# Optimization experiments

Hardware: AMD Instinct MI355X
Metric: run time of the kernel (lower is better)

## Reference

```python
import jax, jax.numpy as jnp
import numpy as np
import math

N_ITERS = 10
N_SPIXELS = 256
NEG_INF = -1e10


def _grid_layout(h, w, n_spixels):
    # init_grid: near-square superpixel grid
    nw = int(math.sqrt(n_spixels * w / h))
    nh = int(math.sqrt(n_spixels * h / w))
    cy = np.minimum((np.arange(h) * nh) // h, nh - 1)
    cx = np.minimum((np.arange(w) * nw) // w, nw - 1)
    iy = np.broadcast_to(cy[:, None], (h, w))
    ix = np.broadcast_to(cx[None, :], (h, w))
    init_idx = iy * nw + ix  # [h,w] hard grid assignment
    # 9 candidate superpixels per pixel (3x3 neighborhood of its grid cell)
    offs = np.array([(dy, dx) for dy in (-1, 0, 1) for dx in (-1, 0, 1)])
    ny = iy[None] + offs[:, 0, None, None]  # [9,h,w]
    nx = ix[None] + offs[:, 1, None, None]
    valid = (ny >= 0) & (ny < nh) & (nx >= 0) & (nx < nw)
    nidx = np.clip(ny, 0, nh - 1) * nw + np.clip(nx, 0, nw - 1)
    return init_idx.astype(np.int32), nidx.astype(np.int32), valid, nw, nh


def setup_inputs() -> dict:
    key = jax.random.key(0)
    x = jax.random.normal(key, (2, 20, 512, 512), dtype=jnp.float32)
    return {"x": x}


def reference(x):
    b, c, h, w = x.shape
    init_idx_np, nidx_np, valid_np, nw, nh = _grid_layout(h, w, N_SPIXELS)
    K = nw * nh
    n = h * w
    init_idx = jnp.asarray(init_idx_np.reshape(n))          # [N]
    nidx = jnp.asarray(nidx_np.reshape(9, n))                # [9,N]
    valid = jnp.asarray(valid_np.reshape(9, n))              # [9,N]
    flat_nidx = nidx.reshape(-1)                             # [9N]

    pf_all = x.reshape(b, c, n)

    def init_spf(pf):  # pf [c,N] -> [c,K]: hard-assignment mean (InitSpixelFeats)
        s = jax.ops.segment_sum(pf.T, init_idx, num_segments=K)      # [K,c]
        cnt = jax.ops.segment_sum(jnp.ones((n,), pf.dtype), init_idx, num_segments=K)
        return (s / jnp.maximum(cnt, 1.0)[:, None]).T

    def calc_neg_dist(pf, spf):  # CalcAssoc: [9,N] neg sq dist to 9 neighbors
        nf = spf[:, nidx]                                    # [c,9,N]
        d = jnp.sum((pf[:, None, :] - nf) ** 2, axis=0)      # [9,N]
        return jnp.where(valid, -d, NEG_INF)

    def map_p2sp(pf, Q):  # CalcSpixelFeats: Q-weighted scatter mean, Q [9,N]
        wf = (pf[:, None, :] * Q[None]).reshape(c, -1)       # [c,9N]
        num = jax.ops.segment_sum(wf.T, flat_nidx, num_segments=K)   # [K,c]
        den = jax.ops.segment_sum(Q.reshape(-1), flat_nidx, num_segments=K)
        return (num / jnp.maximum(den, 1e-8)[:, None]).T

    def per_sample(pf):
        spf0 = init_spf(jax.lax.stop_gradient(pf))  # spf init from detached pf
        Q0 = jnp.zeros((9, n), pf.dtype)
        def body(carry, _):
            spf, _ = carry
            Q = jax.nn.softmax(calc_neg_dist(pf, spf), axis=0)
            return (map_p2sp(pf, Q), Q), None
        (spf, Q), _ = jax.lax.scan(body, (spf0, Q0), None, length=N_ITERS)
        return Q, spf

    Q, spf = jax.vmap(per_sample)(pf_all)
    return Q.reshape(b, 9, h, w), spf, x
```

## Files before the change

### kernel.cpp

```cpp
#include <hip/hip_runtime.h>

#define BATCH 2
#define C 20
#define H 512
#define W 512
#define NPIX (H*W)
#define NW 16
#define NH 16
#define K 256
#define NITERS 10
#define SPLIT 4
#define PITCH 260
#define NEG_INF_F (-1.0e10f)
#define PART_STRIDE 189

__global__ __launch_bounds__(256)
void ssn_init_kernel(const float* __restrict__ x,
                     float* __restrict__ outX,
                     float* __restrict__ wpart) {
    __shared__ float pf_tile[C][PITCH];
    __shared__ float chpart[80];
    int t = threadIdx.x;
    int bi = blockIdx.x;
    int s    = bi & 3;
    int cell = (bi >> 2) & (K - 1);
    int b    = bi >> 10;
    int ky = cell >> 4, kx = cell & 15;
    int py = t >> 5, px = t & 31;
    int y  = ky * 32 + s * 8 + py;
    int xx = kx * 32 + px;

    const float* xb = x    + (size_t)b * C * NPIX + y * W + xx;
    float*       ox = outX + (size_t)b * C * NPIX + y * W + xx;
#pragma unroll
    for (int ch = 0; ch < C; ++ch) {
        float v = xb[(size_t)ch * NPIX];
        ox[(size_t)ch * NPIX] = v;
        pf_tile[ch][t] = v;
    }
    __syncthreads();
    if (t < 80) {
        int ch = t >> 2, q = t & 3;
        const float4* p = (const float4*)&pf_tile[ch][0];
        float s4 = 0.f;
#pragma unroll
        for (int i = 0; i < 16; ++i) {
            float4 v = p[q * 16 + i];
            s4 += v.x + v.y + v.z + v.w;
        }
        chpart[t] = s4;
    }
    __syncthreads();
    if (t < PART_STRIDE) {
        float v = 0.f;
        if (t >= 84 && t < 104) {
            int ch = t - 84;
            v = chpart[ch * 4] + chpart[ch * 4 + 1]
              + chpart[ch * 4 + 2] + chpart[ch * 4 + 3];
        } else if (t == 104) {
            v = 256.0f;
        }
        wpart[(size_t)(b * K + cell) * (SPLIT * PART_STRIDE)
              + s * PART_STRIDE + t] = v;
    }
}

__global__ void ssn_reduce_kernel(const float* __restrict__ part,
                                  float* __restrict__ spf,
                                  float* __restrict__ outSpf,
                                  int final_mode) {
    int idx = blockIdx.x * blockDim.x + threadIdx.x;
    if (idx >= BATCH * K * C) return;
    int ch = idx % C;
    int k  = (idx / C) % K;
    int b  = idx / (C * K);
    int ky = k >> 4, kx = k & 15;
    float num = 0.f, den = 0.f;
#pragma unroll
    for (int j2 = 0; j2 < 9; ++j2) {
        int cy = ky - (j2 / 3 - 1), cx = kx - (j2 % 3 - 1);
        if (cy >= 0 && cy < NH && cx >= 0 && cx < NW) {
            const float* p = part +
                (size_t)(b * K + cy * NW + cx) * (SPLIT * PART_STRIDE) + j2 * 21;
#pragma unroll
            for (int ss = 0; ss < SPLIT; ++ss) {
                num += p[ss * PART_STRIDE + ch];
                den += p[ss * PART_STRIDE + 20];
            }
        }
    }
    float v = num / fmaxf(den, 1e-8f);
    if (final_mode) outSpf[(b * C + ch) * K + k] = v;
    else            spf[(b * K + k) * C + ch]    = v;
}

__global__ __launch_bounds__(256)
void ssn_iterate_kernel(const float* __restrict__ x,
                        const float* __restrict__ spf,
                        float* __restrict__ wpart,
                        float* __restrict__ outQ,
                        int last) {
    __shared__ float spf_lds[9][C];
    __shared__ float sumsq_lds[9];
    __shared__ float pf_tile[C + 1][PITCH];
    __shared__ float w_tile[9][PITCH];

    int t = threadIdx.x;
    int bi = blockIdx.x;
    int s    = bi & 3;
    int cell = (bi >> 2) & (K - 1);
    int b    = bi >> 10;
    int ky = cell >> 4, kx = cell & 15;

    int py = t >> 5, px = t & 31;
    int y  = ky * 32 + s * 8 + py;
    int xx = kx * 32 + px;

    float pf[C];
    const float* xb = x + (size_t)b * C * NPIX + y * W + xx;
#pragma unroll
    for (int ch = 0; ch < C; ++ch) pf[ch] = xb[(size_t)ch * NPIX];

    if (t < 9 * C) {
        int jj = t / C, ch = t % C;
        int ny = ky + jj / 3 - 1, nx = kx + jj % 3 - 1;
        float v = 0.f;
        if (ny >= 0 && ny < NH && nx >= 0 && nx < NW)
            v = spf[(size_t)(b * K + ny * NW + nx) * C + ch];
        spf_lds[jj][ch] = v;
    }
    if (t < 9) {
        int ny = ky + t / 3 - 1, nx = kx + t % 3 - 1;
        float ss2 = 0.f;
        if (ny >= 0 && ny < NH && nx >= 0 && nx < NW) {
            const float* sp = spf + (size_t)(b * K + ny * NW + nx) * C;
#pragma unroll
            for (int ch = 0; ch < C; ++ch) ss2 += sp[ch] * sp[ch];
        }
        sumsq_lds[t] = ss2;
    }
    __syncthreads();

    float sc[9];
#pragma unroll
    for (int j = 0; j < 9; ++j) {
        int ny = ky + j / 3 - 1, nx = kx + j % 3 - 1;
        bool valid = (ny >= 0 && ny < NH && nx >= 0 && nx < NW);
        float dot = 0.f;
#pragma unroll
        for (int ch = 0; ch < C; ++ch) dot = fmaf(pf[ch], spf_lds[j][ch], dot);
        sc[j] = valid ? fmaf(2.f, dot, -sumsq_lds[j]) : NEG_INF_F;
    }
    float m = sc[0];
#pragma unroll
    for (int j = 1; j < 9; ++j) m = fmaxf(m, sc[j]);
    float wv[9], wsum = 0.f;
#pragma unroll
    for (int j = 0; j < 9; ++j) { wv[j] = __expf(sc[j] - m); wsum += wv[j]; }
    float inv = 1.0f / wsum;
#pragma unroll
    for (int j = 0; j < 9; ++j) { wv[j] *= inv; w_tile[j][t] = wv[j]; }
#pragma unroll
    for (int ch = 0; ch < C; ++ch) pf_tile[ch][t] = pf[ch];
    pf_tile[C][t] = 1.0f;

    if (last) {
        float* q = outQ + (size_t)b * 9 * NPIX + y * W + xx;
#pragma unroll
        for (int j = 0; j < 9; ++j) q[(size_t)j * NPIX] = wv[j];
    }
    __syncthreads();

    if (t < 144) {
        int tile = t >> 4;
        int lane = t & 15;
        int jt = tile / 3;
        int rt = tile % 3;
        float acc[3][7];
#pragma unroll
        for (int jj = 0; jj < 3; ++jj)
#pragma unroll
            for (int rr = 0; rr < 7; ++rr) acc[jj][rr] = 0.f;

#pragma unroll
        for (int cc = 0; cc < 4; ++cc) {
            int c4 = lane + (cc << 4);
            float4 w4[3], f4[7];
#pragma unroll
            for (int jj = 0; jj < 3; ++jj)
                w4[jj] = ((const float4*)&w_tile[3 * jt + jj][0])[c4];
#pragma unroll
            for (int rr = 0; rr < 7; ++rr)
                f4[rr] = ((const float4*)&pf_tile[7 * rt + rr][0])[c4];
#pragma unroll
            for (int jj = 0; jj < 3; ++jj)
#pragma unroll
                for (int rr = 0; rr < 7; ++rr) {
                    acc[jj][rr] = fmaf(w4[jj].x, f4[rr].x, acc[jj][rr]);
                    acc[jj][rr] = fmaf(w4[jj].y, f4[rr].y, acc[jj][rr]);
                    acc[jj][rr] = fmaf(w4[jj].z, f4[rr].z, acc[jj][rr]);
                    acc[jj][rr] = fmaf(w4[jj].w, f4[rr].w, acc[jj][rr]);
                }
        }
#pragma unroll
        for (int off = 8; off >= 1; off >>= 1)
#pragma unroll
            for (int jj = 0; jj < 3; ++jj)
#pragma unroll
                for (int rr = 0; rr < 7; ++rr)
                    acc[jj][rr] += __shfl_down(acc[jj][rr], off);
        if (lane == 0) {
            float* dst = wpart + (size_t)(b * K + cell) * (SPLIT * PART_STRIDE)
                       + s * PART_STRIDE;
#pragma unroll
            for (int jj = 0; jj < 3; ++jj)
#pragma unroll
                for (int rr = 0; rr < 7; ++rr)
                    dst[(3 * jt + jj) * 21 + 7 * rt + rr] = acc[jj][rr];
        }
    }
}

extern "C" void kernel_launch(void* const* d_in, const int* in_sizes, int n_in,
                              void* d_out, int out_size, void* d_ws, size_t ws_size,
                              hipStream_t stream) {
    const float* x = (const float*)d_in[0];
    float* out = (float*)d_out;
    float* outQ   = out;
    float* outSpf = out + (size_t)BATCH * 9 * NPIX;
    float* outX   = outSpf + (size_t)BATCH * C * K;

    float* ws   = (float*)d_ws;
    float* spf  = ws;
    float* part = spf + (size_t)BATCH * K * C;

    ssn_init_kernel<<<BATCH * K * SPLIT, 256, 0, stream>>>(x, outX, part);
    ssn_reduce_kernel<<<160, 64, 0, stream>>>(part, spf, nullptr, 0);

    for (int it = 0; it < NITERS; ++it) {
        ssn_iterate_kernel<<<BATCH * K * SPLIT, 256, 0, stream>>>(
            x, spf, part, outQ, (it == NITERS - 1) ? 1 : 0);
        if (it < NITERS - 1)
            ssn_reduce_kernel<<<160, 64, 0, stream>>>(part, spf, nullptr, 0);
    }
    ssn_reduce_kernel<<<160, 64, 0, stream>>>(part, nullptr, outSpf, 1);
}
```

Before: 255.5 us.

## Fuse spixel reduction into iterate kernel via atomics and triple-buffered partials

Removes the separate reduce kernel between iterations. Each iterate block now gathers the 9x9 neighbour partial sums and divides them itself to rebuild its superpixel features. Split blocks accumulate into one record per cell with atomicAdd, and a rotating triple buffer lets each pass zero the buffer used two passes later. The init kernel now covers a whole cell per block, and the final kernel reads a single record instead of four splits. This saves about nine launches and a global round trip per iteration, at the cost of redundant gather work in every block and atomic contention.

```diff
diff --git a/kernel.cpp b/kernel.cpp
--- a/kernel.cpp
+++ b/kernel.cpp
@@ -2,42 +2,50 @@
 
 #define BATCH 2
 #define C 20
-#define H 512
 #define W 512
-#define NPIX (H*W)
+#define NPIX (512*512)
 #define NW 16
 #define NH 16
 #define K 256
 #define NITERS 10
-#define SPLIT 4
 #define PITCH 260
 #define NEG_INF_F (-1.0e10f)
-#define PART_STRIDE 189
+#define REC 189
 
 __global__ __launch_bounds__(256)
 void ssn_init_kernel(const float* __restrict__ x,
                      float* __restrict__ outX,
-                     float* __restrict__ wpart) {
+                     float* __restrict__ bufA,
+                     float* __restrict__ bufB) {
     __shared__ float pf_tile[C][PITCH];
     __shared__ float chpart[80];
-    int t = threadIdx.x;
-    int bi = blockIdx.x;
-    int s    = bi & 3;
-    int cell = (bi >> 2) & (K - 1);
-    int b    = bi >> 10;
-    int ky = cell >> 4, kx = cell & 15;
-    int py = t >> 5, px = t & 31;
-    int y  = ky * 32 + s * 8 + py;
-    int xx = kx * 32 + px;
-
-    const float* xb = x    + (size_t)b * C * NPIX + y * W + xx;
-    float*       ox = outX + (size_t)b * C * NPIX + y * W + xx;
-#pragma unroll
-    for (int ch = 0; ch < C; ++ch) {
-        float v = xb[(size_t)ch * NPIX];
-        ox[(size_t)ch * NPIX] = v;
-        pf_tile[ch][t] = v;
-    }
+    const int t    = threadIdx.x;
+    const int bi   = blockIdx.x;
+    const int cell = bi & (K - 1);
+    const int b    = bi >> 8;
+    const int ky = cell >> 4, kx = cell & 15;
+    const int py = t >> 5, px = t & 31;
+    const int xcol = kx * 32 + px;
+
+    const float* xb = x    + (size_t)b * C * NPIX;
+    float*       ox = outX + (size_t)b * C * NPIX;
+    float sum4[C];
+#pragma unroll
+    for (int ch = 0; ch < C; ++ch) sum4[ch] = 0.f;
+#pragma unroll
+    for (int p = 0; p < 4; ++p) {
+        int y = ky * 32 + p * 8 + py;
+        const float* src = xb + (size_t)y * W + xcol;
+        float*       dst = ox + (size_t)y * W + xcol;
+#pragma unroll
+        for (int ch = 0; ch < C; ++ch) {
+            float v = src[(size_t)ch * NPIX];
+            sum4[ch] += v;
+            dst[(size_t)ch * NPIX] = v;
+        }
+    }
+#pragma unroll
+    for (int ch = 0; ch < C; ++ch) pf_tile[ch][t] = sum4[ch];
     __syncthreads();
     if (t < 80) {
         int ch = t >> 2, q = t & 3;
@@ -51,24 +59,181 @@
         chpart[t] = s4;
     }
     __syncthreads();
-    if (t < PART_STRIDE) {
+    if (t < REC) {
         float v = 0.f;
         if (t >= 84 && t < 104) {
             int ch = t - 84;
             v = chpart[ch * 4] + chpart[ch * 4 + 1]
               + chpart[ch * 4 + 2] + chpart[ch * 4 + 3];
         } else if (t == 104) {
-            v = 256.0f;
-        }
-        wpart[(size_t)(b * K + cell) * (SPLIT * PART_STRIDE)
-              + s * PART_STRIDE + t] = v;
-    }
-}
-
-__global__ void ssn_reduce_kernel(const float* __restrict__ part,
-                                  float* __restrict__ spf,
-                                  float* __restrict__ outSpf,
-                                  int final_mode) {
+            v = 1024.0f;
+        }
+        bufA[(size_t)bi * REC + t] = v;
+        bufB[(size_t)bi * REC + t] = 0.f;
+    }
+}
+
+__global__ __launch_bounds__(256)
+void ssn_iterate_kernel(const float* __restrict__ x,
+                        const float* __restrict__ rp,
+                        float* __restrict__ wp,
+                        float* __restrict__ zp,
+                        float* __restrict__ outQ,
+                        int last) {
+    __shared__ float spf_lds[9][C];
+    __shared__ float den_lds[9];
+    __shared__ float sumsq_lds[9];
+    __shared__ float pf_tile[C][PITCH];
+    __shared__ float w_tile[9][PITCH];
+
+    const int t  = threadIdx.x;
+    const int bi = blockIdx.x;
+    const int s    = bi & 3;
+    const int cell = (bi >> 2) & (K - 1);
+    const int b    = bi >> 10;
+    const int bcell = (b << 8) + cell;
+    const int ky = cell >> 4, kx = cell & 15;
+    const int py = t >> 5, px = t & 31;
+    const int y  = ky * 32 + s * 8 + py;
+    const int xcol = kx * 32 + px;
+
+    if (s == 0 && t < REC) zp[(size_t)bcell * REC + t] = 0.f;
+
+    float pf[C];
+    const float* xb = x + (size_t)b * C * NPIX + (size_t)y * W + xcol;
+#pragma unroll
+    for (int ch = 0; ch < C; ++ch) pf[ch] = xb[(size_t)ch * NPIX];
+
+    float numreg = 0.f;
+    if (t < 180) {
+        int jj = t / 20, ch = t % 20;
+        int ny = ky + jj / 3 - 1, nx = kx + jj % 3 - 1;
+        if (ny >= 0 && ny < NH && nx >= 0 && nx < NW) {
+#pragma unroll
+            for (int j2 = 0; j2 < 9; ++j2) {
+                int cy = ny - (j2 / 3 - 1), cx = nx - (j2 % 3 - 1);
+                if (cy >= 0 && cy < NH && cx >= 0 && cx < NW)
+                    numreg += rp[(size_t)((b << 8) + cy * NW + cx) * REC
+                                 + j2 * 21 + ch];
+            }
+        }
+    }
+    if (t >= 192 && t < 201) {
+        int jj = t - 192;
+        int ny = ky + jj / 3 - 1, nx = kx + jj % 3 - 1;
+        float den = 0.f;
+        if (ny >= 0 && ny < NH && nx >= 0 && nx < NW) {
+#pragma unroll
+            for (int j2 = 0; j2 < 9; ++j2) {
+                int cy = ny - (j2 / 3 - 1), cx = nx - (j2 % 3 - 1);
+                if (cy >= 0 && cy < NH && cx >= 0 && cx < NW)
+                    den += rp[(size_t)((b << 8) + cy * NW + cx) * REC
+                              + j2 * 21 + 20];
+            }
+        }
+        den_lds[jj] = den;
+    }
+    __syncthreads();
+    if (t < 180) {
+        int jj = t / 20, ch = t % 20;
+        spf_lds[jj][ch] = numreg / fmaxf(den_lds[jj], 1e-8f);
+    }
+    __syncthreads();
+    if (t < 9) {
+        float ss2 = 0.f;
+#pragma unroll
+        for (int ch = 0; ch < C; ++ch) ss2 += spf_lds[t][ch] * spf_lds[t][ch];
+        sumsq_lds[t] = ss2;
+    }
+    __syncthreads();
+
+    float sc[9];
+#pragma unroll
+    for (int j = 0; j < 9; ++j) {
+        int ny = ky + j / 3 - 1, nx = kx + j % 3 - 1;
+        bool valid = (ny >= 0 && ny < NH && nx >= 0 && nx < NW);
+        float dot = 0.f;
+#pragma unroll
+        for (int ch = 0; ch < C; ++ch) dot = fmaf(pf[ch], spf_lds[j][ch], dot);
+        sc[j] = valid ? fmaf(2.f, dot, -sumsq_lds[j]) : NEG_INF_F;
+    }
+    float m = sc[0];
+#pragma unroll
+    for (int j = 1; j < 9; ++j) m = fmaxf(m, sc[j]);
+    float wv[9], wsum = 0.f;
+#pragma unroll
+    for (int j = 0; j < 9; ++j) { wv[j] = __expf(sc[j] - m); wsum += wv[j]; }
+    float inv = 1.0f / wsum;
+#pragma unroll
+    for (int j = 0; j < 9; ++j) { wv[j] *= inv; w_tile[j][t] = wv[j]; }
+#pragma unroll
+    for (int ch = 0; ch < C; ++ch) pf_tile[ch][t] = pf[ch];
+
+    if (last) {
+        float* q = outQ + (size_t)b * 9 * NPIX + (size_t)y * W + xcol;
+#pragma unroll
+        for (int j = 0; j < 9; ++j) q[(size_t)j * NPIX] = wv[j];
+    }
+    __syncthreads();
+
+    if (t < 144) {
+        const int tile = t >> 4, lane = t & 15;
+        const int jt = tile / 3, rt = tile % 3;
+        float acc[3][7];
+#pragma unroll
+        for (int jj = 0; jj < 3; ++jj)
+#pragma unroll
+            for (int rr = 0; rr < 7; ++rr) acc[jj][rr] = 0.f;
+
+#pragma unroll
+        for (int cc = 0; cc < 4; ++cc) {
+            int c4 = lane + (cc << 4);
+            float4 w4[3], f4[7];
+#pragma unroll
+            for (int jj = 0; jj < 3; ++jj)
+                w4[jj] = ((const float4*)&w_tile[3 * jt + jj][0])[c4];
+#pragma unroll
+            for (int rr = 0; rr < 7; ++rr) {
+                int r = 7 * rt + rr;
+                if (r < 20) f4[rr] = ((const float4*)&pf_tile[r][0])[c4];
+            }
+#pragma unroll
+            for (int jj = 0; jj < 3; ++jj)
+#pragma unroll
+                for (int rr = 0; rr < 7; ++rr) {
+                    int r = 7 * rt + rr;
+                    if (r < 20) {
+                        acc[jj][rr] = fmaf(w4[jj].x, f4[rr].x, acc[jj][rr]);
+                        acc[jj][rr] = fmaf(w4[jj].y, f4[rr].y, acc[jj][rr]);
+                        acc[jj][rr] = fmaf(w4[jj].z, f4[rr].z, acc[jj][rr]);
+                        acc[jj][rr] = fmaf(w4[jj].w, f4[rr].w, acc[jj][rr]);
+                    } else {
+                        acc[jj][rr] += w4[jj].x + w4[jj].y
+                                     + w4[jj].z + w4[jj].w;
+                    }
+                }
+        }
+#pragma unroll
+        for (int off = 8; off >= 1; off >>= 1)
+#pragma unroll
+            for (int jj = 0; jj < 3; ++jj)
+#pragma unroll
+                for (int rr = 0; rr < 7; ++rr)
+                    acc[jj][rr] += __shfl_down(acc[jj][rr], off);
+        if (lane == 0) {
+            float* dst = wp + (size_t)bcell * REC;
+#pragma unroll
+            for (int jj = 0; jj < 3; ++jj)
+#pragma unroll
+                for (int rr = 0; rr < 7; ++rr)
+                    atomicAdd(&dst[(3 * jt + jj) * 21 + 7 * rt + rr],
+                              acc[jj][rr]);
+        }
+    }
+}
+
+__global__ void ssn_final_kernel(const float* __restrict__ rec,
+                                 float* __restrict__ outSpf) {
     int idx = blockIdx.x * blockDim.x + threadIdx.x;
     if (idx >= BATCH * K * C) return;
     int ch = idx % C;
@@ -80,145 +245,13 @@
     for (int j2 = 0; j2 < 9; ++j2) {
         int cy = ky - (j2 / 3 - 1), cx = kx - (j2 % 3 - 1);
         if (cy >= 0 && cy < NH && cx >= 0 && cx < NW) {
-            const float* p = part +
-                (size_t)(b * K + cy * NW + cx) * (SPLIT * PART_STRIDE) + j2 * 21;
-#pragma unroll
-            for (int ss = 0; ss < SPLIT; ++ss) {
-                num += p[ss * PART_STRIDE + ch];
-                den += p[ss * PART_STRIDE + 20];
-            }
-        }
-    }
-    float v = num / fmaxf(den, 1e-8f);
-    if (final_mode) outSpf[(b * C + ch) * K + k] = v;
-    else            spf[(b * K + k) * C + ch]    = v;
-}
-
-__global__ __launch_bounds__(256)
-void ssn_iterate_kernel(const float* __restrict__ x,
-                        const float* __restrict__ spf,
-                        float* __restrict__ wpart,
-                        float* __restrict__ outQ,
-                        int last) {
-    __shared__ float spf_lds[9][C];
-    __shared__ float sumsq_lds[9];
-    __shared__ float pf_tile[C + 1][PITCH];
-    __shared__ float w_tile[9][PITCH];
-
-    int t = threadIdx.x;
-    int bi = blockIdx.x;
-    int s    = bi & 3;
-    int cell = (bi >> 2) & (K - 1);
-    int b    = bi >> 10;
-    int ky = cell >> 4, kx = cell & 15;
-
-    int py = t >> 5, px = t & 31;
-    int y  = ky * 32 + s * 8 + py;
-    int xx = kx * 32 + px;
-
-    float pf[C];
-    const float* xb = x + (size_t)b * C * NPIX + y * W + xx;
-#pragma unroll
-    for (int ch = 0; ch < C; ++ch) pf[ch] = xb[(size_t)ch * NPIX];
-
-    if (t < 9 * C) {
-        int jj = t / C, ch = t % C;
-        int ny = ky + jj / 3 - 1, nx = kx + jj % 3 - 1;
-        float v = 0.f;
-        if (ny >= 0 && ny < NH && nx >= 0 && nx < NW)
-            v = spf[(size_t)(b * K + ny * NW + nx) * C + ch];
-        spf_lds[jj][ch] = v;
-    }
-    if (t < 9) {
-        int ny = ky + t / 3 - 1, nx = kx + t % 3 - 1;
-        float ss2 = 0.f;
-        if (ny >= 0 && ny < NH && nx >= 0 && nx < NW) {
-            const float* sp = spf + (size_t)(b * K + ny * NW + nx) * C;
-#pragma unroll
-            for (int ch = 0; ch < C; ++ch) ss2 += sp[ch] * sp[ch];
-        }
-        sumsq_lds[t] = ss2;
-    }
-    __syncthreads();
-
-    float sc[9];
-#pragma unroll
-    for (int j = 0; j < 9; ++j) {
-        int ny = ky + j / 3 - 1, nx = kx + j % 3 - 1;
-        bool valid = (ny >= 0 && ny < NH && nx >= 0 && nx < NW);
-        float dot = 0.f;
-#pragma unroll
-        for (int ch = 0; ch < C; ++ch) dot = fmaf(pf[ch], spf_lds[j][ch], dot);
-        sc[j] = valid ? fmaf(2.f, dot, -sumsq_lds[j]) : NEG_INF_F;
-    }
-    float m = sc[0];
-#pragma unroll
-    for (int j = 1; j < 9; ++j) m = fmaxf(m, sc[j]);
-    float wv[9], wsum = 0.f;
-#pragma unroll
-    for (int j = 0; j < 9; ++j) { wv[j] = __expf(sc[j] - m); wsum += wv[j]; }
-    float inv = 1.0f / wsum;
-#pragma unroll
-    for (int j = 0; j < 9; ++j) { wv[j] *= inv; w_tile[j][t] = wv[j]; }
-#pragma unroll
-    for (int ch = 0; ch < C; ++ch) pf_tile[ch][t] = pf[ch];
-    pf_tile[C][t] = 1.0f;
-
-    if (last) {
-        float* q = outQ + (size_t)b * 9 * NPIX + y * W + xx;
-#pragma unroll
-        for (int j = 0; j < 9; ++j) q[(size_t)j * NPIX] = wv[j];
-    }
-    __syncthreads();
-
-    if (t < 144) {
-        int tile = t >> 4;
-        int lane = t & 15;
-        int jt = tile / 3;
-        int rt = tile % 3;
-        float acc[3][7];
-#pragma unroll
-        for (int jj = 0; jj < 3; ++jj)
-#pragma unroll
-            for (int rr = 0; rr < 7; ++rr) acc[jj][rr] = 0.f;
-
-#pragma unroll
-        for (int cc = 0; cc < 4; ++cc) {
-            int c4 = lane + (cc << 4);
-            float4 w4[3], f4[7];
-#pragma unroll
-            for (int jj = 0; jj < 3; ++jj)
-                w4[jj] = ((const float4*)&w_tile[3 * jt + jj][0])[c4];
-#pragma unroll
-            for (int rr = 0; rr < 7; ++rr)
-                f4[rr] = ((const float4*)&pf_tile[7 * rt + rr][0])[c4];
-#pragma unroll
-            for (int jj = 0; jj < 3; ++jj)
-#pragma unroll
-                for (int rr = 0; rr < 7; ++rr) {
-                    acc[jj][rr] = fmaf(w4[jj].x, f4[rr].x, acc[jj][rr]);
-                    acc[jj][rr] = fmaf(w4[jj].y, f4[rr].y, acc[jj][rr]);
-                    acc[jj][rr] = fmaf(w4[jj].z, f4[rr].z, acc[jj][rr]);
-                    acc[jj][rr] = fmaf(w4[jj].w, f4[rr].w, acc[jj][rr]);
-                }
-        }
-#pragma unroll
-        for (int off = 8; off >= 1; off >>= 1)
-#pragma unroll
-            for (int jj = 0; jj < 3; ++jj)
-#pragma unroll
-                for (int rr = 0; rr < 7; ++rr)
-                    acc[jj][rr] += __shfl_down(acc[jj][rr], off);
-        if (lane == 0) {
-            float* dst = wpart + (size_t)(b * K + cell) * (SPLIT * PART_STRIDE)
-                       + s * PART_STRIDE;
-#pragma unroll
-            for (int jj = 0; jj < 3; ++jj)
-#pragma unroll
-                for (int rr = 0; rr < 7; ++rr)
-                    dst[(3 * jt + jj) * 21 + 7 * rt + rr] = acc[jj][rr];
-        }
-    }
+            const float* p = rec + (size_t)((b << 8) + cy * NW + cx) * REC
+                           + j2 * 21;
+            num += p[ch];
+            den += p[20];
+        }
+    }
+    outSpf[((size_t)b * C + ch) * K + k] = num / fmaxf(den, 1e-8f);
 }
 
 extern "C" void kernel_launch(void* const* d_in, const int* in_sizes, int n_in,
@@ -230,18 +263,21 @@
     float* outSpf = out + (size_t)BATCH * 9 * NPIX;
     float* outX   = outSpf + (size_t)BATCH * C * K;
 
-    float* ws   = (float*)d_ws;
-    float* spf  = ws;
-    float* part = spf + (size_t)BATCH * K * C;
-
-    ssn_init_kernel<<<BATCH * K * SPLIT, 256, 0, stream>>>(x, outX, part);
-    ssn_reduce_kernel<<<160, 64, 0, stream>>>(part, spf, nullptr, 0);
+    float* ws = (float*)d_ws;
+    float* buf[3];
+    buf[0] = ws;
+    buf[1] = buf[0] + (size_t)BATCH * K * REC;
+    buf[2] = buf[1] + (size_t)BATCH * K * REC;
+
+    ssn_init_kernel<<<BATCH * K, 256, 0, stream>>>(x, outX, buf[0], buf[1]);
 
     for (int it = 0; it < NITERS; ++it) {
-        ssn_iterate_kernel<<<BATCH * K * SPLIT, 256, 0, stream>>>(
-            x, spf, part, outQ, (it == NITERS - 1) ? 1 : 0);
-        if (it < NITERS - 1)
-            ssn_reduce_kernel<<<160, 64, 0, stream>>>(part, spf, nullptr, 0);
-    }
-    ssn_reduce_kernel<<<160, 64, 0, stream>>>(part, nullptr, outSpf, 1);
-}
+        const float* rp = buf[it % 3];
+        float*       wp = buf[(it + 1) % 3];
+        float*       zp = buf[(it + 2) % 3];
+        ssn_iterate_kernel<<<BATCH * K * 4, 256, 0, stream>>>(
+            x, rp, wp, zp, outQ, (it == NITERS - 1) ? 1 : 0);
+    }
+    ssn_final_kernel<<<(BATCH * K * C + 255) / 256, 256, 0, stream>>>(
+        buf[1], outSpf);
+}
```

Measured after the change: 402.8 us. 57.7% more time.

## Precompute superpixel squared norms in reduce and read padded spf directly

Applied to the files above, without the earlier changes.

The reduce kernel now runs one block per superpixel. It writes the centroid into a 32-float padded row and also stores its squared norm in that row. The iterate kernel no longer stages 9 neighbour centroids in LDS and no longer recomputes their norms behind a barrier. Each thread reads the padded rows directly, relying on the cache and uniform loads. This removes one __syncthreads and some redundant per-block work, in exchange for more global or scalar loads per thread and more reduce blocks.

```diff
diff --git a/kernel.cpp b/kernel.cpp
--- a/kernel.cpp
+++ b/kernel.cpp
@@ -2,9 +2,8 @@
 
 #define BATCH 2
 #define C 20
-#define H 512
 #define W 512
-#define NPIX (H*W)
+#define NPIX (512*512)
 #define NW 16
 #define NH 16
 #define K 256
@@ -13,6 +12,7 @@
 #define PITCH 260
 #define NEG_INF_F (-1.0e10f)
 #define PART_STRIDE 189
+#define SPFP 32
 
 __global__ __launch_bounds__(256)
 void ssn_init_kernel(const float* __restrict__ x,
@@ -30,8 +30,8 @@
     int y  = ky * 32 + s * 8 + py;
     int xx = kx * 32 + px;
 
-    const float* xb = x    + (size_t)b * C * NPIX + y * W + xx;
-    float*       ox = outX + (size_t)b * C * NPIX + y * W + xx;
+    const float* xb = x    + (size_t)b * C * NPIX + (size_t)y * W + xx;
+    float*       ox = outX + (size_t)b * C * NPIX + (size_t)y * W + xx;
 #pragma unroll
     for (int ch = 0; ch < C; ++ch) {
         float v = xb[(size_t)ch * NPIX];
@@ -65,91 +65,92 @@
     }
 }
 
-__global__ void ssn_reduce_kernel(const float* __restrict__ part,
-                                  float* __restrict__ spf,
-                                  float* __restrict__ outSpf,
-                                  int final_mode) {
-    int idx = blockIdx.x * blockDim.x + threadIdx.x;
-    if (idx >= BATCH * K * C) return;
-    int ch = idx % C;
-    int k  = (idx / C) % K;
-    int b  = idx / (C * K);
-    int ky = k >> 4, kx = k & 15;
-    float num = 0.f, den = 0.f;
-#pragma unroll
-    for (int j2 = 0; j2 < 9; ++j2) {
-        int cy = ky - (j2 / 3 - 1), cx = kx - (j2 % 3 - 1);
-        if (cy >= 0 && cy < NH && cx >= 0 && cx < NW) {
-            const float* p = part +
-                (size_t)(b * K + cy * NW + cx) * (SPLIT * PART_STRIDE) + j2 * 21;
-#pragma unroll
-            for (int ss = 0; ss < SPLIT; ++ss) {
-                num += p[ss * PART_STRIDE + ch];
-                den += p[ss * PART_STRIDE + 20];
+__global__ __launch_bounds__(64)
+void ssn_reduce_kernel(const float* __restrict__ part,
+                       float* __restrict__ spfP,
+                       float* __restrict__ outSpf,
+                       int final_mode) {
+    __shared__ float num_lds[C];
+    __shared__ float den_lds;
+    __shared__ float sq_lds[C];
+    const int t  = threadIdx.x;
+    const int bi = blockIdx.x;
+    const int cell = bi & (K - 1);
+    const int b    = bi >> 8;
+    const int ky = cell >> 4, kx = cell & 15;
+
+    if (t <= C) {
+        float acc = 0.f;
+#pragma unroll
+        for (int j2 = 0; j2 < 9; ++j2) {
+            int cy = ky - (j2 / 3 - 1), cx = kx - (j2 % 3 - 1);
+            if (cy >= 0 && cy < NH && cx >= 0 && cx < NW) {
+                const float* p = part +
+                    (size_t)((b << 8) + cy * NW + cx) * (SPLIT * PART_STRIDE)
+                    + j2 * 21 + t;
+#pragma unroll
+                for (int ss = 0; ss < SPLIT; ++ss) acc += p[ss * PART_STRIDE];
             }
         }
-    }
-    float v = num / fmaxf(den, 1e-8f);
-    if (final_mode) outSpf[(b * C + ch) * K + k] = v;
-    else            spf[(b * K + k) * C + ch]    = v;
+        if (t < C) num_lds[t] = acc;
+        else       den_lds    = acc;
+    }
+    __syncthreads();
+    if (t < C) {
+        float v = num_lds[t] / fmaxf(den_lds, 1e-8f);
+        if (final_mode) {
+            outSpf[((size_t)b * C + t) * K + cell] = v;
+        } else {
+            spfP[(size_t)bi * SPFP + t] = v;
+            sq_lds[t] = v * v;
+        }
+    }
+    __syncthreads();
+    if (!final_mode && t == 0) {
+        float ss2 = 0.f;
+#pragma unroll
+        for (int ch = 0; ch < C; ++ch) ss2 += sq_lds[ch];
+        spfP[(size_t)bi * SPFP + C] = ss2;
+    }
 }
 
 __global__ __launch_bounds__(256)
 void ssn_iterate_kernel(const float* __restrict__ x,
-                        const float* __restrict__ spf,
+                        const float* __restrict__ spfP,
                         float* __restrict__ wpart,
                         float* __restrict__ outQ,
                         int last) {
-    __shared__ float spf_lds[9][C];
-    __shared__ float sumsq_lds[9];
     __shared__ float pf_tile[C + 1][PITCH];
     __shared__ float w_tile[9][PITCH];
 
-    int t = threadIdx.x;
-    int bi = blockIdx.x;
-    int s    = bi & 3;
-    int cell = (bi >> 2) & (K - 1);
-    int b    = bi >> 10;
-    int ky = cell >> 4, kx = cell & 15;
-
-    int py = t >> 5, px = t & 31;
-    int y  = ky * 32 + s * 8 + py;
-    int xx = kx * 32 + px;
+    const int t  = threadIdx.x;
+    const int bi = blockIdx.x;
+    const int s    = bi & 3;
+    const int cell = (bi >> 2) & (K - 1);
+    const int b    = bi >> 10;
+    const int ky = cell >> 4, kx = cell & 15;
+    const int py = t >> 5, px = t & 31;
+    const int y  = ky * 32 + s * 8 + py;
+    const int xx = kx * 32 + px;
 
     float pf[C];
-    const float* xb = x + (size_t)b * C * NPIX + y * W + xx;
+    const float* xb = x + (size_t)b * C * NPIX + (size_t)y * W + xx;
 #pragma unroll
     for (int ch = 0; ch < C; ++ch) pf[ch] = xb[(size_t)ch * NPIX];
 
-    if (t < 9 * C) {
-        int jj = t / C, ch = t % C;
-        int ny = ky + jj / 3 - 1, nx = kx + jj % 3 - 1;
-        float v = 0.f;
-        if (ny >= 0 && ny < NH && nx >= 0 && nx < NW)
-            v = spf[(size_t)(b * K + ny * NW + nx) * C + ch];
-        spf_lds[jj][ch] = v;
-    }
-    if (t < 9) {
-        int ny = ky + t / 3 - 1, nx = kx + t % 3 - 1;
-        float ss2 = 0.f;
+    float sc[9];
+#pragma unroll
+    for (int j = 0; j < 9; ++j) {
+        const int ny = ky + j / 3 - 1, nx = kx + j % 3 - 1;
         if (ny >= 0 && ny < NH && nx >= 0 && nx < NW) {
-            const float* sp = spf + (size_t)(b * K + ny * NW + nx) * C;
-#pragma unroll
-            for (int ch = 0; ch < C; ++ch) ss2 += sp[ch] * sp[ch];
-        }
-        sumsq_lds[t] = ss2;
-    }
-    __syncthreads();
-
-    float sc[9];
-#pragma unroll
-    for (int j = 0; j < 9; ++j) {
-        int ny = ky + j / 3 - 1, nx = kx + j % 3 - 1;
-        bool valid = (ny >= 0 && ny < NH && nx >= 0 && nx < NW);
-        float dot = 0.f;
-#pragma unroll
-        for (int ch = 0; ch < C; ++ch) dot = fmaf(pf[ch], spf_lds[j][ch], dot);
-        sc[j] = valid ? fmaf(2.f, dot, -sumsq_lds[j]) : NEG_INF_F;
+            const float* sp = spfP + (size_t)((b << 8) + ny * NW + nx) * SPFP;
+            float dot = 0.f;
+#pragma unroll
+            for (int ch = 0; ch < C; ++ch) dot = fmaf(pf[ch], sp[ch], dot);
+            sc[j] = fmaf(2.f, dot, -sp[C]);
+        } else {
+            sc[j] = NEG_INF_F;
+        }
     }
     float m = sc[0];
 #pragma unroll
@@ -165,17 +166,15 @@
     pf_tile[C][t] = 1.0f;
 
     if (last) {
-        float* q = outQ + (size_t)b * 9 * NPIX + y * W + xx;
+        float* q = outQ + (size_t)b * 9 * NPIX + (size_t)y * W + xx;
 #pragma unroll
         for (int j = 0; j < 9; ++j) q[(size_t)j * NPIX] = wv[j];
     }
     __syncthreads();
 
     if (t < 144) {
-        int tile = t >> 4;
-        int lane = t & 15;
-        int jt = tile / 3;
-        int rt = tile % 3;
+        const int tile = t >> 4, lane = t & 15;
+        const int jt = tile / 3, rt = tile % 3;
         float acc[3][7];
 #pragma unroll
         for (int jj = 0; jj < 3; ++jj)
@@ -210,7 +209,7 @@
                 for (int rr = 0; rr < 7; ++rr)
                     acc[jj][rr] += __shfl_down(acc[jj][rr], off);
         if (lane == 0) {
-            float* dst = wpart + (size_t)(b * K + cell) * (SPLIT * PART_STRIDE)
+            float* dst = wpart + (size_t)((b << 8) + cell) * (SPLIT * PART_STRIDE)
                        + s * PART_STRIDE;
 #pragma unroll
             for (int jj = 0; jj < 3; ++jj)
@@ -231,17 +230,18 @@
     float* outX   = outSpf + (size_t)BATCH * C * K;
 
     float* ws   = (float*)d_ws;
-    float* spf  = ws;
-    float* part = spf + (size_t)BATCH * K * C;
+    float* part = ws;
+    float* spfP = part + (size_t)BATCH * K * SPLIT * PART_STRIDE;
 
     ssn_init_kernel<<<BATCH * K * SPLIT, 256, 0, stream>>>(x, outX, part);
-    ssn_reduce_kernel<<<160, 64, 0, stream>>>(part, spf, nullptr, 0);
+    ssn_reduce_kernel<<<BATCH * K, 64, 0, stream>>>(part, spfP, nullptr, 0);
 
     for (int it = 0; it < NITERS; ++it) {
         ssn_iterate_kernel<<<BATCH * K * SPLIT, 256, 0, stream>>>(
-            x, spf, part, outQ, (it == NITERS - 1) ? 1 : 0);
+            x, spfP, part, outQ, (it == NITERS - 1) ? 1 : 0);
         if (it < NITERS - 1)
-            ssn_reduce_kernel<<<160, 64, 0, stream>>>(part, spf, nullptr, 0);
-    }
-    ssn_reduce_kernel<<<160, 64, 0, stream>>>(part, nullptr, outSpf, 1);
-}
+            ssn_reduce_kernel<<<BATCH * K, 64, 0, stream>>>(
+                part, spfP, nullptr, 0);
+    }
+    ssn_reduce_kernel<<<BATCH * K, 64, 0, stream>>>(part, nullptr, outSpf, 1);
+}
```

Result: slower. 262.3 us (+2.7%).
